# Optimization experiments

Hardware: AMD Instinct MI355X
Metric: run time of the kernel (lower is better)

The kernel has to match this reference:

```python
import jax, jax.numpy as jnp
import numpy as np


def setup_inputs() -> dict:
    key = jax.random.key(0)
    k1, k2, k3 = jax.random.split(key, 3)
    B, T, H, V = 2, 512, 1024, 50000
    hidden = jax.random.normal(k1, (B, T, H), dtype=jnp.float32)
    W = jax.random.normal(k2, (V, H), dtype=jnp.float32) * 0.02
    labels = jax.random.randint(k3, (B, T), 0, V, dtype=jnp.int64)
    attention_mask = jnp.ones((B, T), dtype=jnp.float32)
    return {"hidden": hidden, "W": W, "labels": labels, "attention_mask": attention_mask}


def reference(hidden, W, labels, attention_mask):
    # classification head: [B,T,H] @ [V,H]^T -> [B,T,V]
    logits = jnp.einsum("bth,vh->btv", hidden, W)

    # BCEWithLogits with one-hot targets: elementwise loss is
    #   max(x,0) - x*t + log1p(exp(-|x|))
    # t is 1 only at (b,t,labels[b,t]) when mask>0 and labels>=0, else 0,
    # so we avoid materializing the (B,T,V) target tensor: the -x*t term
    # reduces to a gather of logits at the label index on valid positions.
    base = jnp.maximum(logits, 0.0) + jnp.log1p(jnp.exp(-jnp.abs(logits)))  # [B,T,V]
    valid = (attention_mask > 0) & (labels >= 0)  # [B,T]
    gathered = jnp.take_along_axis(
        logits, jnp.clip(labels, 0)[..., None].astype(jnp.int32), axis=-1
    )[..., 0]  # [B,T]

    mask = attention_mask  # float [B,T]
    total = jnp.sum(base * mask[..., None]) - jnp.sum(jnp.where(valid, gathered, 0.0) * mask)
    loss = total / jnp.sum(mask)
    return logits, loss
```

## Files before the change

### kernel.cpp

```cpp
#include <hip/hip_runtime.h>
#include <hip/hip_bf16.h>

#define M_DIM 1024
#define K_DIM 1024
#define V_DIM 50000
#define NPAD  50048
#define NBLK  (NPAD / 128)
#define WCONV_BLOCKS 25024
#define ACONV_BLOCKS 512

typedef __attribute__((ext_vector_type(8))) short short8;
typedef __attribute__((ext_vector_type(4))) float floatx4;

__device__ inline unsigned short f32_to_bf16(float f) {
    unsigned int u = __float_as_uint(f);
    u += 0x7FFF + ((u >> 16) & 1);
    return (unsigned short)(u >> 16);
}

__device__ inline void async_copy16(const unsigned short* g, unsigned short* l) {
    __builtin_amdgcn_global_load_lds(
        (const __attribute__((address_space(1))) unsigned int*)g,
        (__attribute__((address_space(3))) unsigned int*)l,
        16, 0, 0);
}

__global__ __launch_bounds__(256) void convert_all_kernel(
    const float* __restrict__ W, const float* __restrict__ hidden,
    unsigned short* __restrict__ Wb, unsigned short* __restrict__ Ab)
{
    const float* src;
    unsigned short* dst;
    size_t n_valid, i;
    if (blockIdx.x < WCONV_BLOCKS) {
        src = W; dst = Wb; n_valid = (size_t)V_DIM * K_DIM;
        i = ((size_t)blockIdx.x * 256 + threadIdx.x) * 8;
    } else {
        src = hidden; dst = Ab; n_valid = (size_t)M_DIM * K_DIM;
        i = ((size_t)(blockIdx.x - WCONV_BLOCKS) * 256 + threadIdx.x) * 8;
    }
    unsigned short h[8];
    if (i < n_valid) {
        const float4* p = (const float4*)(src + i);
        float4 a = p[0], b = p[1];
        h[0] = f32_to_bf16(a.x); h[1] = f32_to_bf16(a.y);
        h[2] = f32_to_bf16(a.z); h[3] = f32_to_bf16(a.w);
        h[4] = f32_to_bf16(b.x); h[5] = f32_to_bf16(b.y);
        h[6] = f32_to_bf16(b.z); h[7] = f32_to_bf16(b.w);
    } else {
        #pragma unroll
        for (int j = 0; j < 8; ++j) h[j] = 0;
    }
    uint4 o;
    o.x = (unsigned)h[0] | ((unsigned)h[1] << 16);
    o.y = (unsigned)h[2] | ((unsigned)h[3] << 16);
    o.z = (unsigned)h[4] | ((unsigned)h[5] << 16);
    o.w = (unsigned)h[6] | ((unsigned)h[7] << 16);
    *(uint4*)(dst + i) = o;
}

__device__ __forceinline__ float bce_base(float x) {
    return fmaxf(x, 0.0f) + __logf(1.0f + __expf(-fabsf(x)));
}

template<bool CHECK>
__device__ __forceinline__ float epilogue_store(
    const floatx4 acc[4][4], float* __restrict__ out,
    const int* __restrict__ lab_s, const float* __restrict__ msk_s,
    int bm, int wm, int col0, int lane)
{
    float lsum = 0.0f;
    #pragma unroll
    for (int mi = 0; mi < 4; ++mi) {
        #pragma unroll
        for (int r = 0; r < 4; ++r) {
            const int trow = wm + mi * 16 + (lane >> 4) * 4 + r;
            const int lab  = lab_s[trow];
            const float m  = msk_s[trow];
            float* orow = out + (size_t)(bm * 128 + trow) * V_DIM;
            #pragma unroll
            for (int ni = 0; ni < 4; ++ni) {
                const int gcol = col0 + ni * 16 + (lane & 15);
                const float x = acc[mi][ni][r];
                if (!CHECK || gcol < V_DIM) {
                    orow[gcol] = x;
                    float c = bce_base(x);
                    if (lab == gcol) c -= x;
                    lsum += c * m;
                }
            }
        }
    }
    return lsum;
}

__global__ __launch_bounds__(256) void gemm_loss_kernel(
    const unsigned short* __restrict__ Ab,
    const unsigned short* __restrict__ Wb,
    const int*            __restrict__ labels,
    const float*          __restrict__ amask,
    float*                __restrict__ out,
    double*               __restrict__ loss_acc)
{
    __shared__ unsigned short As[128 * 32];
    __shared__ unsigned short Bs[128 * 32];
    __shared__ int   lab_s[128];
    __shared__ float msk_s[128];
    __shared__ float wred[4];

    const int tid  = threadIdx.x;
    const int lane = tid & 63;
    const int wave = tid >> 6;
    const int wm   = (wave >> 1) * 64;
    const int wn   = (wave & 1) * 64;
    const int bm   = blockIdx.x;
    const int bn   = blockIdx.y;

    if (tid < 128) {
        lab_s[tid] = labels[bm * 128 + tid];
        msk_s[tid] = amask[bm * 128 + tid];
    }

    floatx4 acc[4][4] = {};

    const int c0 = tid, c1 = tid + 256;
    const unsigned short* gA0 = Ab + (size_t)(bm * 128 + (c0 >> 2)) * K_DIM + (c0 & 3) * 8;
    const unsigned short* gA1 = Ab + (size_t)(bm * 128 + (c1 >> 2)) * K_DIM + (c1 & 3) * 8;
    const unsigned short* gB0 = Wb + (size_t)(bn * 128 + (c0 >> 2)) * K_DIM + (c0 & 3) * 8;
    const unsigned short* gB1 = Wb + (size_t)(bn * 128 + (c1 >> 2)) * K_DIM + (c1 & 3) * 8;
    unsigned short* lA0 = &As[c0 * 8];
    unsigned short* lA1 = &As[c1 * 8];
    unsigned short* lB0 = &Bs[c0 * 8];
    unsigned short* lB1 = &Bs[c1 * 8];

    const int frow = lane & 15;
    const int fk   = (lane >> 4) * 8;

    for (int k0 = 0; k0 < K_DIM; k0 += 32) {
        async_copy16(gA0 + k0, lA0);
        async_copy16(gA1 + k0, lA1);
        async_copy16(gB0 + k0, lB0);
        async_copy16(gB1 + k0, lB1);
        __syncthreads();

        short8 af[4], bfr[4];
        #pragma unroll
        for (int i = 0; i < 4; ++i) {
            af[i]  = *(const short8*)&As[(wm + i * 16 + frow) * 32 + fk];
            bfr[i] = *(const short8*)&Bs[(wn + i * 16 + frow) * 32 + fk];
        }
        #pragma unroll
        for (int mi = 0; mi < 4; ++mi)
            #pragma unroll
            for (int ni = 0; ni < 4; ++ni)
                acc[mi][ni] = __builtin_amdgcn_mfma_f32_16x16x32_bf16(
                    af[mi], bfr[ni], acc[mi][ni], 0, 0, 0);
        __syncthreads();
    }

    const int col0 = bn * 128 + wn;
    float lsum;
    if (bn < NBLK - 1) {
        lsum = epilogue_store<false>(acc, out, lab_s, msk_s, bm, wm, col0, lane);
    } else {
        lsum = epilogue_store<true>(acc, out, lab_s, msk_s, bm, wm, col0, lane);
    }

    #pragma unroll
    for (int off = 32; off > 0; off >>= 1) lsum += __shfl_down(lsum, off);
    if (lane == 0) wred[wave] = lsum;
    __syncthreads();
    if (tid == 0)
        atomicAdd(loss_acc, (double)(wred[0] + wred[1] + wred[2] + wred[3]));
}

__global__ __launch_bounds__(256) void finalize_kernel(
    const float* __restrict__ amask, const double* __restrict__ loss_acc,
    float* __restrict__ out_loss)
{
    __shared__ float red[256];
    float s = 0.0f;
    for (int i = threadIdx.x; i < M_DIM; i += 256) s += amask[i];
    red[threadIdx.x] = s;
    __syncthreads();
    for (int k = 128; k > 0; k >>= 1) {
        if (threadIdx.x < k) red[threadIdx.x] += red[threadIdx.x + k];
        __syncthreads();
    }
    if (threadIdx.x == 0)
        *out_loss = (float)(*loss_acc / (double)red[0]);
}

extern "C" void kernel_launch(void* const* d_in, const int* in_sizes, int n_in,
                              void* d_out, int out_size, void* d_ws, size_t ws_size,
                              hipStream_t stream) {
    const float* hidden = (const float*)d_in[0];
    const float* W      = (const float*)d_in[1];
    const int*   labels = (const int*)d_in[2];
    const float* amask  = (const float*)d_in[3];
    float* out = (float*)d_out;

    unsigned short* Wb = (unsigned short*)d_ws;
    unsigned short* Ab = Wb + (size_t)NPAD * K_DIM;
    double* loss_acc   = (double*)(Ab + (size_t)M_DIM * K_DIM);

    hipMemsetAsync(loss_acc, 0, sizeof(double), stream);

    convert_all_kernel<<<WCONV_BLOCKS + ACONV_BLOCKS, 256, 0, stream>>>(W, hidden, Wb, Ab);

    dim3 grid(M_DIM / 128, NBLK);
    gemm_loss_kernel<<<grid, 256, 0, stream>>>(Ab, Wb, labels, amask, out, loss_acc);

    finalize_kernel<<<1, 256, 0, stream>>>(amask, loss_acc, out + (size_t)M_DIM * V_DIM);
}
```

Measured before the change: 575.2 us.

## Multi-stage async LDS pipeline with swizzle and W-sharing block order

Replaces the single-buffered K loop with a 4-buffer global_load_lds pipeline, prefetching three tiles ahead and keeping one barrier per tile, guarded by explicit vmcnt waits. It XOR-swizzles the LDS k-slices to reduce bank conflicts and raises wave priority around the MFMA block. It also remaps the 1D grid so consecutive blocks share the same W tile across all M tiles, and sets a 2-waves-per-EU occupancy hint. The cost is 4x LDS for the tiles, which may limit occupancy.

```diff
diff --git a/kernel.cpp b/kernel.cpp
--- a/kernel.cpp
+++ b/kernel.cpp
@@ -6,11 +6,15 @@
 #define V_DIM 50000
 #define NPAD  50048
 #define NBLK  (NPAD / 128)
+#define NTILES (K_DIM / 32)
 #define WCONV_BLOCKS 25024
 #define ACONV_BLOCKS 512
 
 typedef __attribute__((ext_vector_type(8))) short short8;
 typedef __attribute__((ext_vector_type(4))) float floatx4;
+
+#define VMCNT(n) asm volatile("s_waitcnt vmcnt(" #n ")" ::: "memory")
+#define CFENCE() asm volatile("" ::: "memory")
 
 __device__ inline unsigned short f32_to_bf16(float f) {
     unsigned int u = __float_as_uint(f);
@@ -94,7 +98,7 @@
     return lsum;
 }
 
-__global__ __launch_bounds__(256) void gemm_loss_kernel(
+__global__ __launch_bounds__(256, 2) void gemm_loss_kernel(
     const unsigned short* __restrict__ Ab,
     const unsigned short* __restrict__ Wb,
     const int*            __restrict__ labels,
@@ -102,8 +106,8 @@
     float*                __restrict__ out,
     double*               __restrict__ loss_acc)
 {
-    __shared__ unsigned short As[128 * 32];
-    __shared__ unsigned short Bs[128 * 32];
+    __shared__ __align__(16) unsigned short As[4][128 * 32];
+    __shared__ __align__(16) unsigned short Bs[4][128 * 32];
     __shared__ int   lab_s[128];
     __shared__ float msk_s[128];
     __shared__ float wred[4];
@@ -113,8 +117,11 @@
     const int wave = tid >> 6;
     const int wm   = (wave >> 1) * 64;
     const int wn   = (wave & 1) * 64;
-    const int bm   = blockIdx.x;
-    const int bn   = blockIdx.y;
+
+    const int lin  = blockIdx.x;
+    const int pair = (lin & 7) * NBLK + (lin >> 3);
+    const int bm   = pair & 7;
+    const int bn   = pair >> 3;
 
     if (tid < 128) {
         lab_s[tid] = labels[bm * 128 + tid];
@@ -124,39 +131,57 @@
     floatx4 acc[4][4] = {};
 
     const int c0 = tid, c1 = tid + 256;
-    const unsigned short* gA0 = Ab + (size_t)(bm * 128 + (c0 >> 2)) * K_DIM + (c0 & 3) * 8;
-    const unsigned short* gA1 = Ab + (size_t)(bm * 128 + (c1 >> 2)) * K_DIM + (c1 & 3) * 8;
-    const unsigned short* gB0 = Wb + (size_t)(bn * 128 + (c0 >> 2)) * K_DIM + (c0 & 3) * 8;
-    const unsigned short* gB1 = Wb + (size_t)(bn * 128 + (c1 >> 2)) * K_DIM + (c1 & 3) * 8;
-    unsigned short* lA0 = &As[c0 * 8];
-    unsigned short* lA1 = &As[c1 * 8];
-    unsigned short* lB0 = &Bs[c0 * 8];
-    unsigned short* lB1 = &Bs[c1 * 8];
+    const int r0 = c0 >> 2, sl0 = c0 & 3;
+    const int r1 = c1 >> 2, sl1 = c1 & 3;
+    const int k0e = (sl0 ^ ((r0 >> 1) & 3)) * 8;
+    const int k1e = (sl1 ^ ((r1 >> 1) & 3)) * 8;
+    const unsigned short* gA0 = Ab + (size_t)(bm * 128 + r0) * K_DIM + k0e;
+    const unsigned short* gA1 = Ab + (size_t)(bm * 128 + r1) * K_DIM + k1e;
+    const unsigned short* gB0 = Wb + (size_t)(bn * 128 + r0) * K_DIM + k0e;
+    const unsigned short* gB1 = Wb + (size_t)(bn * 128 + r1) * K_DIM + k1e;
+
+    #define STAGE(t, b) do { \
+        async_copy16(gA0 + (t) * 32, &As[b][c0 * 8]); \
+        async_copy16(gA1 + (t) * 32, &As[b][c1 * 8]); \
+        async_copy16(gB0 + (t) * 32, &Bs[b][c0 * 8]); \
+        async_copy16(gB1 + (t) * 32, &Bs[b][c1 * 8]); \
+    } while (0)
 
     const int frow = lane & 15;
-    const int fk   = (lane >> 4) * 8;
-
-    for (int k0 = 0; k0 < K_DIM; k0 += 32) {
-        async_copy16(gA0 + k0, lA0);
-        async_copy16(gA1 + k0, lA1);
-        async_copy16(gB0 + k0, lB0);
-        async_copy16(gB1 + k0, lB1);
-        __syncthreads();
-
-        short8 af[4], bfr[4];
-        #pragma unroll
-        for (int i = 0; i < 4; ++i) {
-            af[i]  = *(const short8*)&As[(wm + i * 16 + frow) * 32 + fk];
-            bfr[i] = *(const short8*)&Bs[(wn + i * 16 + frow) * 32 + fk];
-        }
-        #pragma unroll
-        for (int mi = 0; mi < 4; ++mi)
-            #pragma unroll
-            for (int ni = 0; ni < 4; ++ni)
-                acc[mi][ni] = __builtin_amdgcn_mfma_f32_16x16x32_bf16(
-                    af[mi], bfr[ni], acc[mi][ni], 0, 0, 0);
-        __syncthreads();
-    }
+    const int s0   = lane >> 4;
+    const int kswe = (s0 ^ ((frow >> 1) & 3)) * 8;
+
+    #define COMPUTE(b) do { \
+        short8 af[4], bfr[4]; \
+        _Pragma("unroll") \
+        for (int i = 0; i < 4; ++i) { \
+            af[i]  = *(const short8*)&As[b][(wm + i * 16 + frow) * 32 + kswe]; \
+            bfr[i] = *(const short8*)&Bs[b][(wn + i * 16 + frow) * 32 + kswe]; \
+        } \
+        __builtin_amdgcn_s_setprio(1); \
+        _Pragma("unroll") \
+        for (int mi = 0; mi < 4; ++mi) \
+            _Pragma("unroll") \
+            for (int ni = 0; ni < 4; ++ni) \
+                acc[mi][ni] = __builtin_amdgcn_mfma_f32_16x16x32_bf16( \
+                    af[mi], bfr[ni], acc[mi][ni], 0, 0, 0); \
+        __builtin_amdgcn_s_setprio(0); \
+    } while (0)
+
+    STAGE(0, 0); STAGE(1, 1); STAGE(2, 2);
+
+    #pragma unroll
+    for (int t = 0; t < NTILES; ++t) {
+        if (t < NTILES - 2)       VMCNT(8);
+        else if (t == NTILES - 2) VMCNT(4);
+        else                      VMCNT(0);
+        __builtin_amdgcn_s_barrier();
+        CFENCE();
+        if (t + 3 < NTILES) STAGE(t + 3, (t + 3) & 3);
+        COMPUTE(t & 3);
+    }
+    #undef STAGE
+    #undef COMPUTE
 
     const int col0 = bn * 128 + wn;
     float lsum;
@@ -208,8 +233,7 @@
 
     convert_all_kernel<<<WCONV_BLOCKS + ACONV_BLOCKS, 256, 0, stream>>>(W, hidden, Wb, Ab);
 
-    dim3 grid(M_DIM / 128, NBLK);
-    gemm_loss_kernel<<<grid, 256, 0, stream>>>(Ab, Wb, labels, amask, out, loss_acc);
+    gemm_loss_kernel<<<dim3(8 * NBLK), 256, 0, stream>>>(Ab, Wb, labels, amask, out, loss_acc);
 
     finalize_kernel<<<1, 256, 0, stream>>>(amask, loss_acc, out + (size_t)M_DIM * V_DIM);
 }
```

After: 536.0 us. 6.8% less time.

## Restructure GEMM into 256x256 tiles with double-buffered swizzled LDS pipeline

Applied to the files above, without the earlier changes.

Replaces the 128x128 tile GEMM, which used a single-buffer K=32 loop with two barriers per step, with a 512-thread 256x256 tile kernel. It double-buffers K=64 slabs in LDS and uses an XOR-swizzled layout to avoid bank conflicts. Async global-to-LDS copies are interleaved with MFMA quadrants using manual vmcnt waits and barriers, with raised wave priority around the MFMAs. The 1D grid is remapped so blocks sharing W column tiles run close together. Each CU does more arithmetic per loaded byte, at the cost of 128KB of LDS per block, which likely allows only one block per CU. The last tile column also reads W rows past the padded region, and those columns are masked out in the epilogue.

```diff
diff --git a/kernel.cpp b/kernel.cpp
--- a/kernel.cpp
+++ b/kernel.cpp
@@ -5,12 +5,18 @@
 #define K_DIM 1024
 #define V_DIM 50000
 #define NPAD  50048
-#define NBLK  (NPAD / 128)
+#define NT_N  196
+#define NT_M  4
+#define NIT   8
 #define WCONV_BLOCKS 25024
 #define ACONV_BLOCKS 512
 
 typedef __attribute__((ext_vector_type(8))) short short8;
 typedef __attribute__((ext_vector_type(4))) float floatx4;
+
+#define VMCNT(n) asm volatile("s_waitcnt vmcnt(" #n ")" ::: "memory")
+#define BAR()    __builtin_amdgcn_s_barrier()
+#define CF()     asm volatile("" ::: "memory")
 
 __device__ inline unsigned short f32_to_bf16(float f) {
     unsigned int u = __float_as_uint(f);
@@ -65,23 +71,24 @@
 
 template<bool CHECK>
 __device__ __forceinline__ float epilogue_store(
-    const floatx4 acc[4][4], float* __restrict__ out,
+    const floatx4 acc[8][4], float* __restrict__ out,
     const int* __restrict__ lab_s, const float* __restrict__ msk_s,
-    int bm, int wm, int col0, int lane)
+    int bm, int wm8, int wn4, int bn, int lane)
 {
     float lsum = 0.0f;
+    const int l4 = lane >> 4;
     #pragma unroll
-    for (int mi = 0; mi < 4; ++mi) {
+    for (int fi = 0; fi < 8; ++fi) {
         #pragma unroll
         for (int r = 0; r < 4; ++r) {
-            const int trow = wm + mi * 16 + (lane >> 4) * 4 + r;
+            const int trow = (wm8 + fi) * 16 + l4 * 4 + r;
             const int lab  = lab_s[trow];
             const float m  = msk_s[trow];
-            float* orow = out + (size_t)(bm * 128 + trow) * V_DIM;
+            float* orow = out + (size_t)(bm * 256 + trow) * V_DIM;
             #pragma unroll
-            for (int ni = 0; ni < 4; ++ni) {
-                const int gcol = col0 + ni * 16 + (lane & 15);
-                const float x = acc[mi][ni][r];
+            for (int fj = 0; fj < 4; ++fj) {
+                const int gcol = bn * 256 + (wn4 + fj) * 16 + (lane & 15);
+                const float x = acc[fi][fj][r];
                 if (!CHECK || gcol < V_DIM) {
                     orow[gcol] = x;
                     float c = bce_base(x);
@@ -94,7 +101,7 @@
     return lsum;
 }
 
-__global__ __launch_bounds__(256) void gemm_loss_kernel(
+__global__ __launch_bounds__(512, 2) void gemm_loss_kernel(
     const unsigned short* __restrict__ Ab,
     const unsigned short* __restrict__ Wb,
     const int*            __restrict__ labels,
@@ -102,76 +109,170 @@
     float*                __restrict__ out,
     double*               __restrict__ loss_acc)
 {
-    __shared__ unsigned short As[128 * 32];
-    __shared__ unsigned short Bs[128 * 32];
-    __shared__ int   lab_s[128];
-    __shared__ float msk_s[128];
-    __shared__ float wred[4];
+    __shared__ __align__(16) unsigned short As0[256 * 64];
+    __shared__ __align__(16) unsigned short As1[256 * 64];
+    __shared__ __align__(16) unsigned short Bs0[256 * 64];
+    __shared__ __align__(16) unsigned short Bs1[256 * 64];
+    __shared__ int   lab_s[256];
+    __shared__ float msk_s[256];
+    __shared__ float wred[8];
 
     const int tid  = threadIdx.x;
     const int lane = tid & 63;
     const int wave = tid >> 6;
-    const int wm   = (wave >> 1) * 64;
-    const int wn   = (wave & 1) * 64;
-    const int bm   = blockIdx.x;
-    const int bn   = blockIdx.y;
-
-    if (tid < 128) {
-        lab_s[tid] = labels[bm * 128 + tid];
-        msk_s[tid] = amask[bm * 128 + tid];
-    }
-
-    floatx4 acc[4][4] = {};
-
-    const int c0 = tid, c1 = tid + 256;
-    const unsigned short* gA0 = Ab + (size_t)(bm * 128 + (c0 >> 2)) * K_DIM + (c0 & 3) * 8;
-    const unsigned short* gA1 = Ab + (size_t)(bm * 128 + (c1 >> 2)) * K_DIM + (c1 & 3) * 8;
-    const unsigned short* gB0 = Wb + (size_t)(bn * 128 + (c0 >> 2)) * K_DIM + (c0 & 3) * 8;
-    const unsigned short* gB1 = Wb + (size_t)(bn * 128 + (c1 >> 2)) * K_DIM + (c1 & 3) * 8;
-    unsigned short* lA0 = &As[c0 * 8];
-    unsigned short* lA1 = &As[c1 * 8];
-    unsigned short* lB0 = &Bs[c0 * 8];
-    unsigned short* lB1 = &Bs[c1 * 8];
-
-    const int frow = lane & 15;
-    const int fk   = (lane >> 4) * 8;
-
-    for (int k0 = 0; k0 < K_DIM; k0 += 32) {
-        async_copy16(gA0 + k0, lA0);
-        async_copy16(gA1 + k0, lA1);
-        async_copy16(gB0 + k0, lB0);
-        async_copy16(gB1 + k0, lB1);
-        __syncthreads();
-
-        short8 af[4], bfr[4];
-        #pragma unroll
-        for (int i = 0; i < 4; ++i) {
-            af[i]  = *(const short8*)&As[(wm + i * 16 + frow) * 32 + fk];
-            bfr[i] = *(const short8*)&Bs[(wn + i * 16 + frow) * 32 + fk];
-        }
-        #pragma unroll
-        for (int mi = 0; mi < 4; ++mi)
-            #pragma unroll
-            for (int ni = 0; ni < 4; ++ni)
-                acc[mi][ni] = __builtin_amdgcn_mfma_f32_16x16x32_bf16(
-                    af[mi], bfr[ni], acc[mi][ni], 0, 0, 0);
-        __syncthreads();
-    }
-
-    const int col0 = bn * 128 + wn;
+    const int wm8  = (wave >> 2) * 8;
+    const int wn4  = (wave & 3) * 4;
+
+    const int lin  = blockIdx.x;
+    const int pair = (lin & 7) * 98 + (lin >> 3);
+    const int bm   = pair & 3;
+    const int bn   = pair >> 2;
+
+    if (tid < 256) {
+        lab_s[tid] = labels[bm * 256 + tid];
+        msk_s[tid] = amask[bm * 256 + tid];
+    }
+
+    floatx4 acc[8][4] = {};
+
+    const int r0 = tid >> 3;
+    const int sw = (tid & 7) ^ (r0 & 7);
+    const unsigned short* pA = Ab + (size_t)(bm * 256 + r0) * K_DIM + sw * 8;
+    const unsigned short* pB = Wb + (size_t)(bn * 256 + r0) * K_DIM + sw * 8;
+
+    #define STAGE_A(dst, h, t) do { \
+        async_copy16(pA + (size_t)(h) * 131072 + (size_t)(t) * 64,         (dst) + (h) * 8192 + tid * 8); \
+        async_copy16(pA + (size_t)(h) * 131072 + (size_t)(t) * 64 + 65536, (dst) + (h) * 8192 + 4096 + tid * 8); \
+    } while (0)
+    #define STAGE_B(dst, h, t) do { \
+        async_copy16(pB + (size_t)(h) * 131072 + (size_t)(t) * 64,         (dst) + (h) * 8192 + tid * 8); \
+        async_copy16(pB + (size_t)(h) * 131072 + (size_t)(t) * 64 + 65536, (dst) + (h) * 8192 + 4096 + tid * 8); \
+    } while (0)
+
+    const int frowb = (lane & 15) * 128;
+    const int cs0   = (((lane >> 4) ^ (lane & 7)) << 4);
+    const int cs1   = cs0 ^ 64;
+    const char* Ac0 = (const char*)As0;
+    const char* Ac1 = (const char*)As1;
+    const char* Bc0 = (const char*)Bs0;
+    const char* Bc1 = (const char*)Bs1;
+
+    short8 a[4][2], b0[2][2], b1[2][2];
+
+    #define LOAD_A(bufc, QM) do { \
+        _Pragma("unroll") \
+        for (int ii = 0; ii < 4; ++ii) { \
+            const char* _p = (bufc) + (wm8 + (QM) * 4 + ii) * 2048 + frowb; \
+            a[ii][0] = *(const short8*)(_p + cs0); \
+            a[ii][1] = *(const short8*)(_p + cs1); \
+        } } while (0)
+    #define LOAD_B(bufc, QN, bb) do { \
+        _Pragma("unroll") \
+        for (int jj = 0; jj < 2; ++jj) { \
+            const char* _p = (bufc) + (wn4 + (QN) * 2 + jj) * 2048 + frowb; \
+            bb[jj][0] = *(const short8*)(_p + cs0); \
+            bb[jj][1] = *(const short8*)(_p + cs1); \
+        } } while (0)
+    #define MFMA_Q(QM, QN, bb) do { \
+        __builtin_amdgcn_s_setprio(1); \
+        _Pragma("unroll") \
+        for (int ii = 0; ii < 4; ++ii) \
+            _Pragma("unroll") \
+            for (int jj = 0; jj < 2; ++jj) { \
+                acc[(QM)*4+ii][(QN)*2+jj] = __builtin_amdgcn_mfma_f32_16x16x32_bf16( \
+                    a[ii][0], bb[jj][0], acc[(QM)*4+ii][(QN)*2+jj], 0, 0, 0); \
+                acc[(QM)*4+ii][(QN)*2+jj] = __builtin_amdgcn_mfma_f32_16x16x32_bf16( \
+                    a[ii][1], bb[jj][1], acc[(QM)*4+ii][(QN)*2+jj], 0, 0, 0); \
+            } \
+        __builtin_amdgcn_s_setprio(0); \
+    } while (0)
+
+    STAGE_A(As0, 0, 0); STAGE_A(As0, 1, 0);
+    STAGE_B(Bs0, 0, 0); STAGE_B(Bs0, 1, 0);
+    STAGE_A(As1, 0, 1);
+
+    for (int i = 0; i < NIT - 1; ++i) {
+        const int tO = 2 * i + 1, tE2 = 2 * i + 2, tO2 = 2 * i + 3;
+        VMCNT(2); BAR(); CF();
+        STAGE_A(As1, 1, tO);
+        LOAD_A(Ac0, 0); LOAD_B(Bc0, 0, b0);
+        MFMA_Q(0, 0, b0);
+        BAR(); CF();
+        STAGE_B(Bs1, 0, tO);
+        LOAD_B(Bc0, 1, b1);
+        MFMA_Q(0, 1, b1);
+        BAR(); CF();
+        STAGE_B(Bs1, 1, tO);
+        LOAD_A(Ac0, 1);
+        MFMA_Q(1, 0, b0);
+        BAR(); CF();
+        STAGE_A(As0, 0, tE2);
+        MFMA_Q(1, 1, b1);
+        VMCNT(2); BAR(); CF();
+        STAGE_A(As0, 1, tE2);
+        LOAD_A(Ac1, 0); LOAD_B(Bc1, 0, b0);
+        MFMA_Q(0, 0, b0);
+        BAR(); CF();
+        STAGE_B(Bs0, 0, tE2);
+        LOAD_B(Bc1, 1, b1);
+        MFMA_Q(0, 1, b1);
+        BAR(); CF();
+        STAGE_B(Bs0, 1, tE2);
+        LOAD_A(Ac1, 1);
+        MFMA_Q(1, 0, b0);
+        BAR(); CF();
+        STAGE_A(As1, 0, tO2);
+        MFMA_Q(1, 1, b1);
+    }
+    VMCNT(2); BAR(); CF();
+    STAGE_A(As1, 1, 15);
+    LOAD_A(Ac0, 0); LOAD_B(Bc0, 0, b0);
+    MFMA_Q(0, 0, b0);
+    BAR(); CF();
+    STAGE_B(Bs1, 0, 15);
+    LOAD_B(Bc0, 1, b1);
+    MFMA_Q(0, 1, b1);
+    BAR(); CF();
+    STAGE_B(Bs1, 1, 15);
+    LOAD_A(Ac0, 1);
+    MFMA_Q(1, 0, b0);
+    BAR(); CF();
+    MFMA_Q(1, 1, b1);
+    VMCNT(0); BAR(); CF();
+    LOAD_A(Ac1, 0); LOAD_B(Bc1, 0, b0);
+    MFMA_Q(0, 0, b0);
+    BAR(); CF();
+    LOAD_B(Bc1, 1, b1);
+    MFMA_Q(0, 1, b1);
+    BAR(); CF();
+    LOAD_A(Ac1, 1);
+    MFMA_Q(1, 0, b0);
+    BAR(); CF();
+    MFMA_Q(1, 1, b1);
+
+    #undef STAGE_A
+    #undef STAGE_B
+    #undef LOAD_A
+    #undef LOAD_B
+    #undef MFMA_Q
+
     float lsum;
-    if (bn < NBLK - 1) {
-        lsum = epilogue_store<false>(acc, out, lab_s, msk_s, bm, wm, col0, lane);
+    if (bn < NT_N - 1) {
+        lsum = epilogue_store<false>(acc, out, lab_s, msk_s, bm, wm8, wn4, bn, lane);
     } else {
-        lsum = epilogue_store<true>(acc, out, lab_s, msk_s, bm, wm, col0, lane);
+        lsum = epilogue_store<true>(acc, out, lab_s, msk_s, bm, wm8, wn4, bn, lane);
     }
 
     #pragma unroll
     for (int off = 32; off > 0; off >>= 1) lsum += __shfl_down(lsum, off);
     if (lane == 0) wred[wave] = lsum;
     __syncthreads();
-    if (tid == 0)
-        atomicAdd(loss_acc, (double)(wred[0] + wred[1] + wred[2] + wred[3]));
+    if (tid == 0) {
+        double s = 0.0;
+        #pragma unroll
+        for (int w = 0; w < 8; ++w) s += (double)wred[w];
+        atomicAdd(loss_acc, s);
+    }
 }
 
 __global__ __launch_bounds__(256) void finalize_kernel(
@@ -208,8 +309,7 @@
 
     convert_all_kernel<<<WCONV_BLOCKS + ACONV_BLOCKS, 256, 0, stream>>>(W, hidden, Wb, Ab);
 
-    dim3 grid(M_DIM / 128, NBLK);
-    gemm_loss_kernel<<<grid, 256, 0, stream>>>(Ab, Wb, labels, amask, out, loss_acc);
+    gemm_loss_kernel<<<dim3(NT_M * NT_N), 512, 0, stream>>>(Ab, Wb, labels, amask, out, loss_acc);
 
     finalize_kernel<<<1, 256, 0, stream>>>(amask, loss_acc, out + (size_t)M_DIM * V_DIM);
 }
```

Result: faster. 541.7 us (-5.8%).
